# Performance work log

Hardware: AMD Instinct MI355X
Metric: run time of the kernel (lower is better)

The kernel has to match this reference:

```python
import jax, jax.numpy as jnp
import numpy as np

PERIOD = 0.1


def setup_inputs() -> dict:
    key = jax.random.key(0)
    ks = jax.random.split(key, 16)
    B, N, C, P = 2, 3072, 4, 4
    E, H, T, F, L = 512, 8, 256, 64, 4
    Nt = N // P

    def rn(k, shape, scale=0.02):
        return jax.random.normal(k, shape, jnp.float32) * scale

    return {
        "x": jax.random.normal(ks[0], (B, N, C), jnp.float32),
        "t": jax.random.normal(ks[1], (B, T), jnp.float32),
        "vec_map": jax.random.normal(ks[2], (B, N, 3), jnp.float32),
        # RelativeBias dense: freq features -> heads
        "W_rb": rn(ks[3], (F, H)),
        "b_rb": jnp.zeros((H,), jnp.float32),
        # patch embedding dense: P*C -> E
        "W_embed": rn(ks[4], (P * C, E), 0.1),
        "b_embed": jnp.zeros((E,), jnp.float32),
        "pos_emb": rn(ks[5], (Nt, E)),
        # stacked per-block params (leading dim L = n_blocks)
        "ada1_W1": rn(ks[6], (L, T, T)),
        "ada1_b1": jnp.zeros((L, T), jnp.float32),
        "ada1_W2": rn(ks[7], (L, T, 3 * E)),
        "ada1_b2": jnp.zeros((L, 3 * E), jnp.float32),
        "qkv_W": rn(ks[8], (L, E, 3 * E)),
        "qkv_b": jnp.zeros((L, 3 * E), jnp.float32),
        "out_W": rn(ks[9], (L, E, E)),
        "out_b": jnp.zeros((L, E), jnp.float32),
        "ada2_W1": rn(ks[10], (L, T, T)),
        "ada2_b1": jnp.zeros((L, T), jnp.float32),
        "ada2_W2": rn(ks[11], (L, T, 3 * E)),
        "ada2_b2": jnp.zeros((L, 3 * E), jnp.float32),
        "mlp_W1": rn(ks[12], (L, E, 4 * E)),
        "mlp_b1": jnp.zeros((L, 4 * E), jnp.float32),
        "mlp_W2": rn(ks[13], (L, 4 * E, E)),
        "mlp_b2": jnp.zeros((L, E), jnp.float32),
    }


def _layernorm(y):
    # flax LayerNorm(use_bias=False, use_scale=False), eps=1e-6
    mu = jnp.mean(y, axis=-1, keepdims=True)
    var = jnp.mean(jnp.square(y - mu), axis=-1, keepdims=True)
    return (y - mu) * jax.lax.rsqrt(var + 1e-6)


def _adaln(t, W1, b1, W2, b2):
    h = jax.nn.silu(t @ W1 + b1)
    m = (h @ W2 + b2)[..., None, :]  # (B, 1, 3E)
    return jnp.split(m, 3, axis=-1)


def reference(x, t, vec_map, W_rb, b_rb, W_embed, b_embed, pos_emb,
              ada1_W1, ada1_b1, ada1_W2, ada1_b2, qkv_W, qkv_b, out_W, out_b,
              ada2_W1, ada2_b1, ada2_W2, ada2_b2, mlp_W1, mlp_b1, mlp_W2, mlp_b2):
    B, N, C = x.shape
    Nt, E = pos_emb.shape
    P = N // Nt
    F, H = W_rb.shape
    hd = E // H

    # patchify tokens: (B, N, C) -> (B, Nt, P*C); mean vec per patch
    xp = x.reshape(B, Nt, P * C)
    vp = vec_map.reshape(B, Nt, P, 3).mean(axis=-2)

    # relative bias logits (B, Nt, Nt, H)
    v = vp / jnp.linalg.norm(vp, axis=-1, keepdims=True)
    dif = v[..., :, None, :] - v[..., None, :, :]
    dot = 1.0 - 0.5 * jnp.sum(dif * dif, axis=-1)
    angle = jnp.arccos(jnp.clip(dot, -1.0, 1.0)) / 0.005
    freqs = jnp.linspace(0, 1, F // 2) / PERIOD
    ph = freqs * angle[..., None]  # (B, Nt, Nt, F/2)
    pos = jnp.concatenate((jnp.sin(ph), jnp.cos(ph)), axis=-1)
    bias = pos @ W_rb + b_rb

    # patch embed + learned positional embedding
    h0 = xp @ W_embed + b_embed + pos_emb
    inv_sqrt_hd = 1.0 / jnp.sqrt(jnp.float32(hd))

    def block(xc, params):
        (aW1, ab1, aW2, ab2, qW, qb, oW, ob,
         cW1, cb1, cW2, cb2, mW1, mb1, mW2, mb2) = params
        g1, be1, al1 = _adaln(t, aW1, ab1, aW2, ab2)
        y = (g1 + 1.0) * _layernorm(xc) + be1
        qkv = (y @ qW + qb).reshape(B, Nt, H, 3, hd)
        q, k, vv = qkv[..., 0, :], qkv[..., 1, :], qkv[..., 2, :]
        logits = jnp.einsum('bqht,bkht->bqkh', q, k) * inv_sqrt_hd + bias
        logits = logits - jnp.max(logits, axis=-2, keepdims=True)
        attn = jax.nn.softmax(logits, axis=-2)  # softmax over keys (K axis)
        y = jnp.einsum('bqkh,bkht->bqht', attn, vv).reshape(B, Nt, E)
        y = y @ oW + ob
        xc = xc + al1 * y / jnp.sqrt(1.0 + al1 * al1)
        g2, be2, al2 = _adaln(t, cW1, cb1, cW2, cb2)
        y = (g2 + 1.0) * _layernorm(xc) + be2
        y = jax.nn.gelu(y @ mW1 + mb1) @ mW2 + mb2
        xc = xc + al2 * y / jnp.sqrt(1.0 + al2 * al2)
        return xc, None

    params = (ada1_W1, ada1_b1, ada1_W2, ada1_b2, qkv_W, qkv_b, out_W, out_b,
              ada2_W1, ada2_b1, ada2_W2, ada2_b2, mlp_W1, mlp_b1, mlp_W2, mlp_b2)
    out, _ = jax.lax.scan(block, h0, params)
    return out
```

## Files before the change

kernel.cpp:

```cpp
#include <hip/hip_runtime.h>
#include <hip/hip_bf16.h>


#define NT 768
#define EDIM 512
#define E3 1536
#define E4 2048
#define NH 8
#define TB 2

typedef unsigned short ushort_t;
typedef __attribute__((ext_vector_type(8))) short bf16x8;
typedef __attribute__((ext_vector_type(4))) float f32x4;

#define GLOAD(src, dst) __builtin_amdgcn_global_load_lds( \
    (const __attribute__((address_space(1))) unsigned int*)(src), \
    (__attribute__((address_space(3))) unsigned int*)(dst), 16, 0, 0)

__device__ inline float b2f(ushort_t u) {
    unsigned int i = ((unsigned int)u) << 16; float f;
    __builtin_memcpy(&f, &i, 4); return f;
}
__device__ inline ushort_t f2b(float f) {
    __hip_bfloat16 h = __float2bfloat16(f);
    ushort_t u; __builtin_memcpy(&u, &h, 2); return u;
}
__device__ inline float gelu_tanh(float u) {
    float z = 1.5957691216057308f * (u + 0.044715f * u * u * u);
    z = fminf(z, 40.f);
    float t = __expf(z);
    float th = (t - 1.f) / (t + 1.f);
    return 0.5f * u * (1.f + th);
}

__global__ __launch_bounds__(256) void k_bias(const float* __restrict__ vm, const float* __restrict__ W_rb,
                                              const float* __restrict__ b_rb, ushort_t* __restrict__ biasT) {
    int bq = blockIdx.x; int b = bq / NT, q = bq % NT;
    __shared__ float sv[NT * 3];
    int tid = threadIdx.x, lane = tid & 63, wave = tid >> 6;
    for (int i = tid; i < NT; i += 256) {
        const float* vp = vm + ((long)b * 3072 + i * 4) * 3;
        float s0 = vp[0] + vp[3] + vp[6] + vp[9];
        float s1 = vp[1] + vp[4] + vp[7] + vp[10];
        float s2 = vp[2] + vp[5] + vp[8] + vp[11];
        float inv = rsqrtf(s0 * s0 + s1 * s1 + s2 * s2);
        sv[i * 3 + 0] = s0 * inv; sv[i * 3 + 1] = s1 * inv; sv[i * 3 + 2] = s2 * inv;
    }

    int g = lane >> 4, col = lane & 15;
    ushort_t tw[16];
    #pragma unroll
    for (int j = 0; j < 8; ++j) {
        float wsv = (col < 8) ? W_rb[(g * 8 + j) * 8 + col] : 0.f;
        float wcv = (col < 8) ? W_rb[(32 + g * 8 + j) * 8 + col] : 0.f;
        tw[j] = f2b(wsv); tw[8 + j] = f2b(wcv);
    }
    bf16x8 bsf, bcf;
    __builtin_memcpy(&bsf, tw, 16);
    __builtin_memcpy(&bcf, tw + 8, 16);
    float brh = (col < 8) ? b_rb[col] : 0.f;
    __syncthreads();

    float vq0 = sv[q * 3], vq1 = sv[q * 3 + 1], vq2 = sv[q * 3 + 2];
    float gf = (float)(8 * g);

    for (int it = 0; it < 12; ++it) {
        int tile = (it * 4 + wave) * 16;
        int p = tile + col;
        float d0 = vq0 - sv[p * 3], d1 = vq1 - sv[p * 3 + 1], d2 = vq2 - sv[p * 3 + 2];
        float dot = 1.f - 0.5f * (d0 * d0 + d1 * d1 + d2 * d2);
        dot = fminf(1.f, fmaxf(-1.f, dot));
        float theta = acosf(dot) * (2000.f / 31.f);
        float s1, c1; __sincosf(theta, &s1, &c1);
        float sg, cg; __sincosf(theta * gf, &sg, &cg);
        ushort_t fs[16];
        #pragma unroll
        for (int j = 0; j < 8; ++j) {
            fs[j] = f2b(sg); fs[8 + j] = f2b(cg);
            float ns = sg * c1 + cg * s1;
            cg = cg * c1 - sg * s1;
            sg = ns;
        }
        bf16x8 asf, acf;
        __builtin_memcpy(&asf, fs, 16);
        __builtin_memcpy(&acf, fs + 8, 16);
        f32x4 acc = {0.f, 0.f, 0.f, 0.f};
        acc = __builtin_amdgcn_mfma_f32_16x16x32_bf16(asf, bsf, acc, 0, 0, 0);
        acc = __builtin_amdgcn_mfma_f32_16x16x32_bf16(acf, bcf, acc, 0, 0, 0);
        if (col < 8) {
            ushort_t o[4];
            #pragma unroll
            for (int r = 0; r < 4; ++r) o[r] = f2b(acc[r] + brh);
            long off = (long)(b * 8 + col) * NT * NT + (long)q * NT + tile + 4 * g;
            uint2 pk;
            pk.x = (unsigned int)o[0] | ((unsigned int)o[1] << 16);
            pk.y = (unsigned int)o[2] | ((unsigned int)o[3] << 16);
            *(uint2*)(biasT + off) = pk;
        }
    }
}

__global__ __launch_bounds__(256) void k_embedln(const float* __restrict__ x, const float* __restrict__ W,
                                                 const float* __restrict__ be, const float* __restrict__ pe,
                                                 const float* __restrict__ ada,
                                                 float* __restrict__ xc, ushort_t* __restrict__ ln16) {
    int row = blockIdx.x; int nt = row % NT, b = row / NT;
    __shared__ float sx[16];
    __shared__ float sm[8];
    int tid = threadIdx.x, w = tid >> 6;
    if (tid < 16) sx[tid] = x[row * 16 + tid];
    __syncthreads();
    float a0 = be[tid] + pe[nt * EDIM + tid];
    float a1 = be[tid + 256] + pe[nt * EDIM + tid + 256];
    #pragma unroll
    for (int j = 0; j < 16; ++j) {
        a0 += sx[j] * W[j * EDIM + tid];
        a1 += sx[j] * W[j * EDIM + tid + 256];
    }
    xc[(long)row * EDIM + tid] = a0;
    xc[(long)row * EDIM + tid + 256] = a1;
    float s1 = a0 + a1, s2 = a0 * a0 + a1 * a1;
    for (int o = 32; o; o >>= 1) { s1 += __shfl_down(s1, o); s2 += __shfl_down(s2, o); }
    if ((tid & 63) == 0) { sm[w] = s1; sm[4 + w] = s2; }
    __syncthreads();
    s1 = sm[0] + sm[1] + sm[2] + sm[3];
    s2 = sm[4] + sm[5] + sm[6] + sm[7];
    float mu = s1 * (1.f / 512.f);
    float var = s2 * (1.f / 512.f) - mu * mu;
    float inv = rsqrtf(var + 1e-6f);
    const float* ap = ada + (long)b * E3;
    float r0 = (ap[tid] + 1.f) * ((a0 - mu) * inv) + ap[512 + tid];
    float r1 = (ap[tid + 256] + 1.f) * ((a1 - mu) * inv) + ap[512 + tid + 256];
    ln16[(long)row * EDIM + tid] = f2b(r0);
    ln16[(long)row * EDIM + tid + 256] = f2b(r1);
}

__global__ __launch_bounds__(256) void k_adaln(const float* __restrict__ t,
    const float* __restrict__ a1W1, const float* __restrict__ a1b1, const float* __restrict__ a1W2, const float* __restrict__ a1b2,
    const float* __restrict__ a2W1, const float* __restrict__ a2b1, const float* __restrict__ a2W2, const float* __restrict__ a2b2,
    float* __restrict__ ada) {
    int blk = blockIdx.x; int b = blk & 1, lw = blk >> 1; int which = lw & 1, l = lw >> 1;
    const float* W1 = (which ? a2W1 : a1W1) + (long)l * 256 * 256;
    const float* b1 = (which ? a2b1 : a1b1) + l * 256;
    const float* W2 = (which ? a2W2 : a1W2) + (long)l * 256 * E3;
    const float* b2 = (which ? a2b2 : a1b2) + l * E3;
    __shared__ float st[256], sh[256];
    int tid = threadIdx.x;
    st[tid] = t[b * 256 + tid];
    __syncthreads();
    float a = b1[tid];
    for (int i = 0; i < 256; ++i) a += st[i] * W1[i * 256 + tid];
    sh[tid] = a / (1.f + __expf(-a));
    __syncthreads();
    int c = blockIdx.y * 256 + tid;
    float m = b2[c];
    for (int i = 0; i < 256; ++i) m += sh[i] * W2[i * E3 + c];
    ada[(long)(lw * 2 + b) * E3 + c] = m;
}

__global__ __launch_bounds__(256) void k_wTall(
        const float* __restrict__ qkvW, const float* __restrict__ outW,
        const float* __restrict__ m1W, const float* __restrict__ m2W,
        ushort_t* __restrict__ qkvWt, ushort_t* __restrict__ outWt,
        ushort_t* __restrict__ m1Wt, ushort_t* __restrict__ m2Wt) {
    int idx = blockIdx.x, l = blockIdx.y;
    const float* W; ushort_t* Wt; int Kd, Nd, ntile, ktile;
    if (idx < 192)      { W = qkvW; Wt = qkvWt; Kd = 512;  Nd = 1536; ntile = idx % 24; ktile = idx / 24; }
    else if (idx < 256) { W = outW; Wt = outWt; Kd = 512;  Nd = 512;  idx -= 192; ntile = idx % 8;  ktile = idx / 8; }
    else if (idx < 512) { W = m1W;  Wt = m1Wt;  Kd = 512;  Nd = 2048; idx -= 256; ntile = idx % 32; ktile = idx / 32; }
    else                { W = m2W;  Wt = m2Wt;  Kd = 2048; Nd = 512;  idx -= 512; ntile = idx % 8;  ktile = idx / 8; }
    const float* Wp = W + (long)l * Kd * Nd;
    ushort_t* Wtp = Wt + (long)l * Kd * Nd;
    int n0 = ntile * 64, k0 = ktile * 64;
    __shared__ float s[64][65];
    int tid = threadIdx.x;
    #pragma unroll
    for (int it = 0; it < 4; ++it) {
        int i2 = tid + it * 256;
        int r = i2 >> 4, c4 = (i2 & 15) * 4;
        float4 vv = *(const float4*)(Wp + (long)(k0 + r) * Nd + n0 + c4);
        s[r][c4] = vv.x; s[r][c4 + 1] = vv.y; s[r][c4 + 2] = vv.z; s[r][c4 + 3] = vv.w;
    }
    __syncthreads();
    #pragma unroll
    for (int it = 0; it < 4; ++it) {
        int i2 = tid + it * 256;
        int rn = i2 >> 4, ck = (i2 & 15) * 4;
        long base = (long)(n0 + rn) * Kd + k0 + ck;
        #pragma unroll
        for (int j = 0; j < 4; ++j) Wtp[base + j] = f2b(s[ck + j][rn]);
    }
}

__global__ __launch_bounds__(256) void k_attn(const ushort_t* __restrict__ qkv16,
        const ushort_t* __restrict__ vT, const ushort_t* __restrict__ biasT,
        ushort_t* __restrict__ attnb) {
    int qt = blockIdx.x, bh = blockIdx.y;
    int b = bh >> 3, h = bh & 7;
    __shared__ __align__(16) ushort_t Ks[2][4096];
    __shared__ __align__(16) ushort_t Vs[2][4096];
    __shared__ __align__(16) ushort_t Bi[2][4096];
    int tid = threadIdx.x, lane = tid & 63, wave = tid >> 6;
    int g = lane >> 4, c = lane & 15;
    int ls = lane & 7, lr = lane >> 3;
    int stg_col = (ls ^ lr) * 8;
    int q0 = qt * 64;

    bf16x8 aq[2];
    {
        const ushort_t* qp = qkv16 + ((long)(b * NT + q0 + wave * 16 + c) * E3) + h * 192;
        aq[0] = *(const bf16x8*)(qp + g * 8);
        aq[1] = *(const bf16x8*)(qp + 32 + g * 8);
    }
    float m_r[4], l_r[4];
    f32x4 o_acc[4];
    #pragma unroll
    for (int rr = 0; rr < 4; ++rr) { m_r[rr] = -1e30f; l_r[rr] = 0.f; }
    #pragma unroll
    for (int nf = 0; nf < 4; ++nf) o_acc[nf] = f32x4{0.f, 0.f, 0.f, 0.f};

#define STAGEA(buf, kt) { \
        int k0_ = (kt) * 64; \
        _Pragma("unroll") \
        for (int is = 0; is < 2; ++is) { \
            int row = is * 32 + wave * 8 + lr; \
            int dstb = (is * 32 + wave * 8) * 64; \
            GLOAD(qkv16 + (long)(b * NT + k0_ + row) * E3 + h * 192 + 64 + stg_col, &Ks[buf][dstb]); \
            GLOAD(vT + ((long)bh * 64 + row) * NT + k0_ + stg_col, &Vs[buf][dstb]); \
            GLOAD(biasT + (long)bh * NT * NT + (long)(q0 + row) * NT + k0_ + ls * 8, &Bi[buf][dstb]); \
        } }

    STAGEA(0, 0);
    __syncthreads();
    int cur = 0;
    for (int kt = 0; kt < 12; ++kt) {
        if (kt + 1 < 12) STAGEA(cur ^ 1, kt + 1);
        f32x4 s[4];
        __builtin_amdgcn_s_setprio(1);
        #pragma unroll
        for (int nf = 0; nf < 4; ++nf) {
            s[nf] = f32x4{0.f, 0.f, 0.f, 0.f};
            #pragma unroll
            for (int kh = 0; kh < 2; ++kh) {
                int row = nf * 16 + c;
                bf16x8 bk = *(const bf16x8*)(&Ks[cur][row * 64 + (((kh * 4 + g) ^ (row & 7))) * 8]);
                s[nf] = __builtin_amdgcn_mfma_f32_16x16x32_bf16(aq[kh], bk, s[nf], 0, 0, 0);
            }
        }
        __builtin_amdgcn_s_setprio(0);
        float p[4][4], mt[4];
        #pragma unroll
        for (int rr = 0; rr < 4; ++rr) {
            int ql = wave * 16 + g * 4 + rr;
            #pragma unroll
            for (int nf = 0; nf < 4; ++nf)
                p[nf][rr] = s[nf][rr] * 0.125f + b2f(Bi[cur][ql * 64 + nf * 16 + c]);
            float mx = fmaxf(fmaxf(p[0][rr], p[1][rr]), fmaxf(p[2][rr], p[3][rr]));
            mx = fmaxf(mx, __shfl_xor(mx, 1));
            mx = fmaxf(mx, __shfl_xor(mx, 2));
            mx = fmaxf(mx, __shfl_xor(mx, 4));
            mx = fmaxf(mx, __shfl_xor(mx, 8));
            mt[rr] = mx;
        }
        #pragma unroll
        for (int rr = 0; rr < 4; ++rr) {
            float mnew = fmaxf(m_r[rr], mt[rr]);
            float sc = __expf(m_r[rr] - mnew);
            m_r[rr] = mnew;
            float rsum = 0.f;
            #pragma unroll
            for (int nf = 0; nf < 4; ++nf) {
                p[nf][rr] = __expf(p[nf][rr] - mnew);
                rsum += p[nf][rr];
            }
            rsum += __shfl_xor(rsum, 1); rsum += __shfl_xor(rsum, 2);
            rsum += __shfl_xor(rsum, 4); rsum += __shfl_xor(rsum, 8);
            l_r[rr] = l_r[rr] * sc + rsum;
            #pragma unroll
            for (int nf = 0; nf < 4; ++nf) o_acc[nf][rr] *= sc;
        }
        #pragma unroll
        for (int nf = 0; nf < 4; ++nf) {
            int kl = nf * 16 + c;
            int slot = kl >> 3, win = kl & 7;
            #pragma unroll
            for (int rr = 0; rr < 4; ++rr) {
                int ql = wave * 16 + g * 4 + rr;
                Bi[cur][ql * 64 + ((slot ^ (ql & 7)) * 8) + win] = f2b(p[nf][rr]);
            }
        }
        asm volatile("s_waitcnt lgkmcnt(0)" ::: "memory");
        bf16x8 ap[2];
        #pragma unroll
        for (int kh = 0; kh < 2; ++kh) {
            int ql = wave * 16 + c;
            ap[kh] = *(const bf16x8*)(&Bi[cur][ql * 64 + (((kh * 4 + g) ^ (ql & 7))) * 8]);
        }
        __builtin_amdgcn_s_setprio(1);
        #pragma unroll
        for (int nf = 0; nf < 4; ++nf) {
            #pragma unroll
            for (int kh = 0; kh < 2; ++kh) {
                int row = nf * 16 + c;
                bf16x8 bv = *(const bf16x8*)(&Vs[cur][row * 64 + (((kh * 4 + g) ^ (row & 7))) * 8]);
                o_acc[nf] = __builtin_amdgcn_mfma_f32_16x16x32_bf16(ap[kh], bv, o_acc[nf], 0, 0, 0);
            }
        }
        __builtin_amdgcn_s_setprio(0);
        __syncthreads();
        cur ^= 1;
    }
#undef STAGEA
    #pragma unroll
    for (int nf = 0; nf < 4; ++nf) {
        #pragma unroll
        for (int rr = 0; rr < 4; ++rr) {
            int ql = wave * 16 + g * 4 + rr;
            Ks[0][ql * 64 + nf * 16 + c] = f2b(o_acc[nf][rr] / l_r[rr]);
        }
    }
    asm volatile("s_waitcnt lgkmcnt(0)" ::: "memory");
    __syncthreads();
    int orow = wave * 16 + (lane >> 2);
    int ocol = (lane & 3) * 16;
    const ushort_t* srcO = &Ks[0][orow * 64 + ocol];
    ushort_t* dstO = attnb + (long)(b * NT + q0 + orow) * EDIM + h * 64 + ocol;
    *(bf16x8*)(dstO) = *(const bf16x8*)(srcO);
    *(bf16x8*)(dstO + 8) = *(const bf16x8*)(srcO + 8);
}

template<int EPI>
__global__ __launch_bounds__(256) void k_mm64(
        const ushort_t* __restrict__ A0, const ushort_t* __restrict__ B0,
        const float* __restrict__ bias, void* __restrict__ C0,
        int Kchunk, int lda, int ldb, int ldc, ushort_t* __restrict__ vTout) {
    __shared__ __align__(16) ushort_t As[2][4096];
    __shared__ __align__(16) ushort_t Bs[2][4096];
    int tid = threadIdx.x, lane = tid & 63, wave = tid >> 6;
    int wm = wave >> 1, wn = wave & 1;
    int m0 = blockIdx.y * 64, n0 = blockIdx.x * 64;
    int lr = lane >> 3, ls = lane & 7;
    int stg_col = (ls ^ lr) * 8;
    int r = lane & 15, g = lane >> 4, rs = r & 7;
    int nt = Kchunk >> 6;
    const ushort_t* A = A0 + (long)blockIdx.z * Kchunk;
    const ushort_t* B = B0 + (long)blockIdx.z * Kchunk;

    f32x4 acc[2][2];
    #pragma unroll
    for (int i = 0; i < 2; ++i)
        #pragma unroll
        for (int j = 0; j < 2; ++j) acc[i][j] = f32x4{0.f, 0.f, 0.f, 0.f};

#define STAGE64(buf, t) { \
        int k0_ = (t) * 64; \
        _Pragma("unroll") \
        for (int c0 = 0; c0 < 4; ++c0) { \
            int ch = wave * 4 + c0; \
            if (ch < 8) { \
                GLOAD(A + (long)(m0 + ch * 8 + lr) * lda + k0_ + stg_col, &As[buf][ch * 512]); \
            } else { \
                GLOAD(B + (long)(n0 + (ch - 8) * 8 + lr) * ldb + k0_ + stg_col, &Bs[buf][(ch - 8) * 512]); \
            } \
        } }

    STAGE64(0, 0);
    __syncthreads();
    int cur = 0;
    for (int t = 0; t < nt; ++t) {
        if (t + 1 < nt) STAGE64(cur ^ 1, t + 1);
        bf16x8 af[2][2], bfr[2][2];
        #pragma unroll
        for (int i = 0; i < 2; ++i) {
            int row = wm * 32 + i * 16 + r;
            #pragma unroll
            for (int kh = 0; kh < 2; ++kh)
                af[i][kh] = *(const bf16x8*)(&As[cur][row * 64 + (((kh * 4 + g) ^ rs)) * 8]);
        }
        #pragma unroll
        for (int j = 0; j < 2; ++j) {
            int row = wn * 32 + j * 16 + r;
            #pragma unroll
            for (int kh = 0; kh < 2; ++kh)
                bfr[j][kh] = *(const bf16x8*)(&Bs[cur][row * 64 + (((kh * 4 + g) ^ rs)) * 8]);
        }
        #pragma unroll
        for (int kh = 0; kh < 2; ++kh)
            #pragma unroll
            for (int i = 0; i < 2; ++i)
                #pragma unroll
                for (int j = 0; j < 2; ++j)
                    acc[i][j] = __builtin_amdgcn_mfma_f32_16x16x32_bf16(af[i][kh], bfr[j][kh], acc[i][j], 0, 0, 0);
        __syncthreads();
        cur ^= 1;
    }
#undef STAGE64

    int gr4 = g * 4, cL = lane & 15;
    if constexpr (EPI == 0 || EPI == 1) {
        ushort_t* C = (ushort_t*)C0;
        #pragma unroll
        for (int i = 0; i < 2; ++i) {
            int mrow = m0 + wm * 32 + i * 16 + gr4;
            #pragma unroll
            for (int j = 0; j < 2; ++j) {
                int n = n0 + wn * 32 + j * 16 + cL;
                float bn = bias[n];
                ushort_t o[4];
                #pragma unroll
                for (int rr = 0; rr < 4; ++rr) {
                    float vv = acc[i][j][rr] + bn;
                    if constexpr (EPI == 1) vv = gelu_tanh(vv);
                    o[rr] = f2b(vv);
                    C[(long)(mrow + rr) * ldc + n] = o[rr];
                }
                if constexpr (EPI == 0) {
                    if (vTout) {
                        int seg = n % 192;
                        if (seg >= 128) {
                            int h = n / 192, d = seg - 128;
                            int b2 = (mrow >= NT) ? 1 : 0;
                            int tok = mrow - b2 * NT;
                            uint2 pk;
                            pk.x = (unsigned int)o[0] | ((unsigned int)o[1] << 16);
                            pk.y = (unsigned int)o[2] | ((unsigned int)o[3] << 16);
                            *(uint2*)(vTout + ((long)((b2 * 8 + h) * 64 + d)) * NT + tok) = pk;
                        }
                    }
                }
            }
        }
    } else {
        float* C = (float*)C0 + (long)blockIdx.z * (1536 * 512);
        #pragma unroll
        for (int i = 0; i < 2; ++i) {
            int mrow = m0 + wm * 32 + i * 16 + gr4;
            #pragma unroll
            for (int j = 0; j < 2; ++j) {
                int n = n0 + wn * 32 + j * 16 + cL;
                #pragma unroll
                for (int rr = 0; rr < 4; ++rr)
                    C[(long)(mrow + rr) * ldc + n] = acc[i][j][rr];
            }
        }
    }
}

__global__ __launch_bounds__(256) void k_redln(const float* __restrict__ P, int kSplit,
        const float* __restrict__ bias, const float* __restrict__ ada,
        int lw_res, int lw_next,
        const float* __restrict__ xin, float* __restrict__ xout,
        ushort_t* __restrict__ lnout) {
    int tid = threadIdx.x;
    int row = blockIdx.x * 2 + (tid >> 7);
    int col = (tid & 127) * 4;
    int b = (row >= NT) ? 1 : 0;
    long idx = (long)row * EDIM + col;
    float4 s = *(const float4*)(P + idx);
    for (int kc = 1; kc < kSplit; ++kc) {
        float4 p = *(const float4*)(P + (long)kc * (1536 * 512) + idx);
        s.x += p.x; s.y += p.y; s.z += p.z; s.w += p.w;
    }
    float4 bv = *(const float4*)(bias + col);
    const float* al = ada + (long)(lw_res * 2 + b) * E3 + 1024;
    float4 av = *(const float4*)(al + col);
    float4 xv = *(const float4*)(xin + idx);
    float4 r;
    r.x = xv.x + av.x * rsqrtf(1.f + av.x * av.x) * (s.x + bv.x);
    r.y = xv.y + av.y * rsqrtf(1.f + av.y * av.y) * (s.y + bv.y);
    r.z = xv.z + av.z * rsqrtf(1.f + av.z * av.z) * (s.z + bv.z);
    r.w = xv.w + av.w * rsqrtf(1.f + av.w * av.w) * (s.w + bv.w);
    *(float4*)(xout + idx) = r;

    if (lnout) {
        float s1 = r.x + r.y + r.z + r.w;
        float s2 = r.x * r.x + r.y * r.y + r.z * r.z + r.w * r.w;
        for (int o = 32; o; o >>= 1) { s1 += __shfl_xor(s1, o); s2 += __shfl_xor(s2, o); }
        __shared__ float sm[8];
        int w = tid >> 6;
        if ((tid & 63) == 0) { sm[w] = s1; sm[4 + w] = s2; }
        __syncthreads();
        int p2 = (tid >> 7) * 2;
        s1 = sm[p2] + sm[p2 + 1];
        s2 = sm[4 + p2] + sm[4 + p2 + 1];
        float mu = s1 * (1.f / 512.f);
        float var = s2 * (1.f / 512.f) - mu * mu;
        float inv = rsqrtf(var + 1e-6f);
        const float* ap = ada + (long)(lw_next * 2 + b) * E3;
        float4 gv = *(const float4*)(ap + col);
        float4 bev = *(const float4*)(ap + 512 + col);
        ushort_t o4[4];
        o4[0] = f2b((gv.x + 1.f) * ((r.x - mu) * inv) + bev.x);
        o4[1] = f2b((gv.y + 1.f) * ((r.y - mu) * inv) + bev.y);
        o4[2] = f2b((gv.z + 1.f) * ((r.z - mu) * inv) + bev.z);
        o4[3] = f2b((gv.w + 1.f) * ((r.w - mu) * inv) + bev.w);
        uint2 pk;
        pk.x = (unsigned int)o4[0] | ((unsigned int)o4[1] << 16);
        pk.y = (unsigned int)o4[2] | ((unsigned int)o4[3] << 16);
        *(uint2*)(lnout + idx) = pk;
    }
}

extern "C" void kernel_launch(void* const* d_in, const int* in_sizes, int n_in,
                              void* d_out, int out_size, void* d_ws, size_t ws_size,
                              hipStream_t stream) {
    const float* x       = (const float*)d_in[0];
    const float* t       = (const float*)d_in[1];
    const float* vec_map = (const float*)d_in[2];
    const float* W_rb    = (const float*)d_in[3];
    const float* b_rb    = (const float*)d_in[4];
    const float* W_embed = (const float*)d_in[5];
    const float* b_embed = (const float*)d_in[6];
    const float* pos_emb = (const float*)d_in[7];
    const float* a1W1    = (const float*)d_in[8];
    const float* a1b1    = (const float*)d_in[9];
    const float* a1W2    = (const float*)d_in[10];
    const float* a1b2    = (const float*)d_in[11];
    const float* qkv_W   = (const float*)d_in[12];
    const float* qkv_b   = (const float*)d_in[13];
    const float* out_W   = (const float*)d_in[14];
    const float* out_b   = (const float*)d_in[15];
    const float* a2W1    = (const float*)d_in[16];
    const float* a2b1    = (const float*)d_in[17];
    const float* a2W2    = (const float*)d_in[18];
    const float* a2b2    = (const float*)d_in[19];
    const float* mlp_W1  = (const float*)d_in[20];
    const float* mlp_b1  = (const float*)d_in[21];
    const float* mlp_W2  = (const float*)d_in[22];
    const float* mlp_b2  = (const float*)d_in[23];

    float* ws = (float*)d_ws;
    size_t o = 0;
    ushort_t* biasT = (ushort_t*)(ws + o); o += 4718592;
    float* ada      = ws + o; o += 24576;
    float* xc       = ws + o; o += 786432;
    ushort_t* ln16  = (ushort_t*)(ws + o); o += 393216;
    ushort_t* qkv16 = (ushort_t*)(ws + o); o += 1179648;
    ushort_t* vT    = (ushort_t*)(ws + o); o += 393216;
    ushort_t* attnb = (ushort_t*)(ws + o); o += 393216;
    ushort_t* mlph  = (ushort_t*)(ws + o); o += 1572864;
    ushort_t* qkvWt = (ushort_t*)(ws + o); o += 1572864;
    ushort_t* outWt = (ushort_t*)(ws + o); o += 524288;
    ushort_t* mlp1Wt = (ushort_t*)(ws + o); o += 2097152;
    ushort_t* mlp2Wt = (ushort_t*)(ws + o); o += 2097152;
    float* P        = ws + o; o += 3145728;

    k_adaln<<<dim3(16, 6), 256, 0, stream>>>(t, a1W1, a1b1, a1W2, a1b2, a2W1, a2b1, a2W2, a2b2, ada);
    k_bias<<<TB * NT, 256, 0, stream>>>(vec_map, W_rb, b_rb, biasT);
    k_embedln<<<TB * NT, 256, 0, stream>>>(x, W_embed, b_embed, pos_emb, ada, xc, ln16);
    k_wTall<<<dim3(768, 4), 256, 0, stream>>>(qkv_W, out_W, mlp_W1, mlp_W2,
                                              qkvWt, outWt, mlp1Wt, mlp2Wt);

    for (int l = 0; l < 4; ++l) {
        int lw0 = l * 2, lw1 = l * 2 + 1;
        k_mm64<0><<<dim3(24, 24, 1), 256, 0, stream>>>(
            ln16, qkvWt + (long)l * 786432, qkv_b + l * E3,
            qkv16, 512, 512, 512, E3, vT);
        k_attn<<<dim3(12, 16), 256, 0, stream>>>(qkv16, vT, biasT, attnb);
        k_mm64<4><<<dim3(8, 24, 2), 256, 0, stream>>>(
            attnb, outWt + (long)l * 262144, nullptr,
            P, 256, 512, 512, EDIM, nullptr);
        k_redln<<<768, 256, 0, stream>>>(P, 2, out_b + l * EDIM, ada, lw0, lw1, xc, xc, ln16);
        k_mm64<1><<<dim3(32, 24, 1), 256, 0, stream>>>(
            ln16, mlp1Wt + (long)l * 1048576, mlp_b1 + l * E4,
            mlph, 512, 512, 512, E4, nullptr);
        k_mm64<4><<<dim3(8, 24, 4), 256, 0, stream>>>(
            mlph, mlp2Wt + (long)l * 1048576, nullptr,
            P, 512, 2048, 2048, EDIM, nullptr);
        k_redln<<<768, 256, 0, stream>>>(P, 4, mlp_b2 + l * EDIM, ada, lw1, lw1 + 1,
            xc, (l == 3) ? (float*)d_out : xc, (l == 3) ? nullptr : ln16);
    }
}
```

Before: 347.0 us.

## Use 128x64 tiles for QKV/MLP1 GEMMs and 32-query attention blocks

Adds a dedicated k_mmA kernel with 128-row M tiles (each wave computing 32x64) for the QKV and MLP-up GEMMs, which raises per-block reuse of A/B tiles and halves the grid. The split-K GEMMs move to a simplified k_mm64p kernel. Attention now uses 2-wave blocks handling 32 queries each, doubling the block count to improve occupancy across CUs while re-staging K/V twice as often. Fewer GEMM blocks may leave CUs underused, and the added accumulators raise register pressure.

After: 370.1 us. +6.7%, slower.

```diff
diff --git a/kernel.cpp b/kernel.cpp
--- a/kernel.cpp
+++ b/kernel.cpp
@@ -192,19 +192,19 @@
     }
 }
 
-__global__ __launch_bounds__(256) void k_attn(const ushort_t* __restrict__ qkv16,
+__global__ __launch_bounds__(128) void k_attn(const ushort_t* __restrict__ qkv16,
         const ushort_t* __restrict__ vT, const ushort_t* __restrict__ biasT,
         ushort_t* __restrict__ attnb) {
     int qt = blockIdx.x, bh = blockIdx.y;
     int b = bh >> 3, h = bh & 7;
     __shared__ __align__(16) ushort_t Ks[2][4096];
     __shared__ __align__(16) ushort_t Vs[2][4096];
-    __shared__ __align__(16) ushort_t Bi[2][4096];
+    __shared__ __align__(16) ushort_t Bi[2][2048];
     int tid = threadIdx.x, lane = tid & 63, wave = tid >> 6;
     int g = lane >> 4, c = lane & 15;
     int ls = lane & 7, lr = lane >> 3;
     int stg_col = (ls ^ lr) * 8;
-    int q0 = qt * 64;
+    int q0 = qt * 32;
 
     bf16x8 aq[2];
     {
@@ -222,12 +222,16 @@
 #define STAGEA(buf, kt) { \
         int k0_ = (kt) * 64; \
         _Pragma("unroll") \
-        for (int is = 0; is < 2; ++is) { \
-            int row = is * 32 + wave * 8 + lr; \
-            int dstb = (is * 32 + wave * 8) * 64; \
-            GLOAD(qkv16 + (long)(b * NT + k0_ + row) * E3 + h * 192 + 64 + stg_col, &Ks[buf][dstb]); \
-            GLOAD(vT + ((long)bh * 64 + row) * NT + k0_ + stg_col, &Vs[buf][dstb]); \
-            GLOAD(biasT + (long)bh * NT * NT + (long)(q0 + row) * NT + k0_ + ls * 8, &Bi[buf][dstb]); \
+        for (int c0 = 0; c0 < 4; ++c0) { \
+            int ch = wave * 4 + c0; \
+            int row = ch * 8 + lr; \
+            GLOAD(qkv16 + (long)(b * NT + k0_ + row) * E3 + h * 192 + 64 + stg_col, &Ks[buf][ch * 512]); \
+            GLOAD(vT + ((long)bh * 64 + row) * NT + k0_ + stg_col, &Vs[buf][ch * 512]); \
+        } \
+        _Pragma("unroll") \
+        for (int c0 = 0; c0 < 2; ++c0) { \
+            int ch = wave * 2 + c0; \
+            GLOAD(biasT + (long)bh * NT * NT + (long)(q0 + ch * 8 + lr) * NT + k0_ + ls * 8, &Bi[buf][ch * 512]); \
         } }
 
     STAGEA(0, 0);
@@ -330,10 +334,105 @@
 }
 
 template<int EPI>
-__global__ __launch_bounds__(256) void k_mm64(
+__global__ __launch_bounds__(256) void k_mmA(
         const ushort_t* __restrict__ A0, const ushort_t* __restrict__ B0,
-        const float* __restrict__ bias, void* __restrict__ C0,
-        int Kchunk, int lda, int ldb, int ldc, ushort_t* __restrict__ vTout) {
+        const float* __restrict__ bias, ushort_t* __restrict__ C,
+        int lda, int ldb, int ldc, ushort_t* __restrict__ vTout) {
+    __shared__ __align__(16) ushort_t As[2][8192];
+    __shared__ __align__(16) ushort_t Bs[2][4096];
+    int tid = threadIdx.x, lane = tid & 63, wave = tid >> 6;
+    int m0 = blockIdx.y * 128, n0 = blockIdx.x * 64;
+    int lr = lane >> 3, ls = lane & 7;
+    int stg_col = (ls ^ lr) * 8;
+    int r = lane & 15, g = lane >> 4, rs = r & 7;
+
+    f32x4 acc[2][4];
+    #pragma unroll
+    for (int i = 0; i < 2; ++i)
+        #pragma unroll
+        for (int j = 0; j < 4; ++j) acc[i][j] = f32x4{0.f, 0.f, 0.f, 0.f};
+
+#define STAGEM(buf, t) { \
+        int k0_ = (t) * 64; \
+        _Pragma("unroll") \
+        for (int c0 = 0; c0 < 6; ++c0) { \
+            int ch = wave * 6 + c0; \
+            if (ch < 16) { \
+                GLOAD(A0 + (long)(m0 + ch * 8 + lr) * lda + k0_ + stg_col, &As[buf][ch * 512]); \
+            } else { \
+                GLOAD(B0 + (long)(n0 + (ch - 16) * 8 + lr) * ldb + k0_ + stg_col, &Bs[buf][(ch - 16) * 512]); \
+            } \
+        } }
+
+    STAGEM(0, 0);
+    __syncthreads();
+    int cur = 0;
+    for (int t = 0; t < 8; ++t) {
+        if (t + 1 < 8) STAGEM(cur ^ 1, t + 1);
+        bf16x8 af[2][2], bfr[4][2];
+        #pragma unroll
+        for (int i = 0; i < 2; ++i) {
+            int row = wave * 32 + i * 16 + r;
+            #pragma unroll
+            for (int kh = 0; kh < 2; ++kh)
+                af[i][kh] = *(const bf16x8*)(&As[cur][row * 64 + (((kh * 4 + g) ^ rs)) * 8]);
+        }
+        #pragma unroll
+        for (int j = 0; j < 4; ++j) {
+            int row = j * 16 + r;
+            #pragma unroll
+            for (int kh = 0; kh < 2; ++kh)
+                bfr[j][kh] = *(const bf16x8*)(&Bs[cur][row * 64 + (((kh * 4 + g) ^ rs)) * 8]);
+        }
+        #pragma unroll
+        for (int kh = 0; kh < 2; ++kh)
+            #pragma unroll
+            for (int i = 0; i < 2; ++i)
+                #pragma unroll
+                for (int j = 0; j < 4; ++j)
+                    acc[i][j] = __builtin_amdgcn_mfma_f32_16x16x32_bf16(af[i][kh], bfr[j][kh], acc[i][j], 0, 0, 0);
+        __syncthreads();
+        cur ^= 1;
+    }
+#undef STAGEM
+
+    int gr4 = g * 4, cL = lane & 15;
+    #pragma unroll
+    for (int i = 0; i < 2; ++i) {
+        int mrow = m0 + wave * 32 + i * 16 + gr4;
+        #pragma unroll
+        for (int j = 0; j < 4; ++j) {
+            int n = n0 + j * 16 + cL;
+            float bn = bias[n];
+            ushort_t o[4];
+            #pragma unroll
+            for (int rr = 0; rr < 4; ++rr) {
+                float vv = acc[i][j][rr] + bn;
+                if constexpr (EPI == 1) vv = gelu_tanh(vv);
+                o[rr] = f2b(vv);
+                C[(long)(mrow + rr) * ldc + n] = o[rr];
+            }
+            if constexpr (EPI == 0) {
+                if (vTout) {
+                    int seg = n % 192;
+                    if (seg >= 128) {
+                        int h = n / 192, d = seg - 128;
+                        int b2 = (mrow >= NT) ? 1 : 0;
+                        int tok = mrow - b2 * NT;
+                        uint2 pk;
+                        pk.x = (unsigned int)o[0] | ((unsigned int)o[1] << 16);
+                        pk.y = (unsigned int)o[2] | ((unsigned int)o[3] << 16);
+                        *(uint2*)(vTout + ((long)((b2 * 8 + h) * 64 + d)) * NT + tok) = pk;
+                    }
+                }
+            }
+        }
+    }
+}
+
+__global__ __launch_bounds__(256) void k_mm64p(
+        const ushort_t* __restrict__ A0, const ushort_t* __restrict__ B0,
+        float* __restrict__ C0, int Kchunk, int lda, int ldb, int ldc) {
     __shared__ __align__(16) ushort_t As[2][4096];
     __shared__ __align__(16) ushort_t Bs[2][4096];
     int tid = threadIdx.x, lane = tid & 63, wave = tid >> 6;
@@ -397,51 +496,16 @@
 #undef STAGE64
 
     int gr4 = g * 4, cL = lane & 15;
-    if constexpr (EPI == 0 || EPI == 1) {
-        ushort_t* C = (ushort_t*)C0;
-        #pragma unroll
-        for (int i = 0; i < 2; ++i) {
-            int mrow = m0 + wm * 32 + i * 16 + gr4;
-            #pragma unroll
-            for (int j = 0; j < 2; ++j) {
-                int n = n0 + wn * 32 + j * 16 + cL;
-                float bn = bias[n];
-                ushort_t o[4];
-                #pragma unroll
-                for (int rr = 0; rr < 4; ++rr) {
-                    float vv = acc[i][j][rr] + bn;
-                    if constexpr (EPI == 1) vv = gelu_tanh(vv);
-                    o[rr] = f2b(vv);
-                    C[(long)(mrow + rr) * ldc + n] = o[rr];
-                }
-                if constexpr (EPI == 0) {
-                    if (vTout) {
-                        int seg = n % 192;
-                        if (seg >= 128) {
-                            int h = n / 192, d = seg - 128;
-                            int b2 = (mrow >= NT) ? 1 : 0;
-                            int tok = mrow - b2 * NT;
-                            uint2 pk;
-                            pk.x = (unsigned int)o[0] | ((unsigned int)o[1] << 16);
-                            pk.y = (unsigned int)o[2] | ((unsigned int)o[3] << 16);
-                            *(uint2*)(vTout + ((long)((b2 * 8 + h) * 64 + d)) * NT + tok) = pk;
-                        }
-                    }
-                }
-            }
-        }
-    } else {
-        float* C = (float*)C0 + (long)blockIdx.z * (1536 * 512);
-        #pragma unroll
-        for (int i = 0; i < 2; ++i) {
-            int mrow = m0 + wm * 32 + i * 16 + gr4;
-            #pragma unroll
-            for (int j = 0; j < 2; ++j) {
-                int n = n0 + wn * 32 + j * 16 + cL;
-                #pragma unroll
-                for (int rr = 0; rr < 4; ++rr)
-                    C[(long)(mrow + rr) * ldc + n] = acc[i][j][rr];
-            }
+    float* C = C0 + (long)blockIdx.z * (1536 * 512);
+    #pragma unroll
+    for (int i = 0; i < 2; ++i) {
+        int mrow = m0 + wm * 32 + i * 16 + gr4;
+        #pragma unroll
+        for (int j = 0; j < 2; ++j) {
+            int n = n0 + wn * 32 + j * 16 + cL;
+            #pragma unroll
+            for (int rr = 0; rr < 4; ++rr)
+                C[(long)(mrow + rr) * ldc + n] = acc[i][j][rr];
         }
     }
 }
@@ -553,20 +617,18 @@
 
     for (int l = 0; l < 4; ++l) {
         int lw0 = l * 2, lw1 = l * 2 + 1;
-        k_mm64<0><<<dim3(24, 24, 1), 256, 0, stream>>>(
+        k_mmA<0><<<dim3(24, 12), 256, 0, stream>>>(
             ln16, qkvWt + (long)l * 786432, qkv_b + l * E3,
-            qkv16, 512, 512, 512, E3, vT);
-        k_attn<<<dim3(12, 16), 256, 0, stream>>>(qkv16, vT, biasT, attnb);
-        k_mm64<4><<<dim3(8, 24, 2), 256, 0, stream>>>(
-            attnb, outWt + (long)l * 262144, nullptr,
-            P, 256, 512, 512, EDIM, nullptr);
+            qkv16, 512, 512, E3, vT);
+        k_attn<<<dim3(24, 16), 128, 0, stream>>>(qkv16, vT, biasT, attnb);
+        k_mm64p<<<dim3(8, 24, 2), 256, 0, stream>>>(
+            attnb, outWt + (long)l * 262144, P, 256, 512, 512, EDIM);
         k_redln<<<768, 256, 0, stream>>>(P, 2, out_b + l * EDIM, ada, lw0, lw1, xc, xc, ln16);
-        k_mm64<1><<<dim3(32, 24, 1), 256, 0, stream>>>(
+        k_mmA<1><<<dim3(32, 12), 256, 0, stream>>>(
             ln16, mlp1Wt + (long)l * 1048576, mlp_b1 + l * E4,
-            mlph, 512, 512, 512, E4, nullptr);
-        k_mm64<4><<<dim3(8, 24, 4), 256, 0, stream>>>(
-            mlph, mlp2Wt + (long)l * 1048576, nullptr,
-            P, 512, 2048, 2048, EDIM, nullptr);
+            mlph, 512, 512, E4, nullptr);
+        k_mm64p<<<dim3(8, 24, 4), 256, 0, stream>>>(
+            mlph, mlp2Wt + (long)l * 1048576, P, 512, 2048, 2048, EDIM);
         k_redln<<<768, 256, 0, stream>>>(P, 4, mlp_b2 + l * EDIM, ada, lw1, lw1 + 1,
             xc, (l == 3) ? (float*)d_out : xc, (l == 3) ? nullptr : ln16);
     }
```
